# Optimization experiments

Measured on AMD Instinct MI355X. Metric: run time of the kernel, lower is better.

The kernel has to match this reference:

```python
import jax, jax.numpy as jnp
import numpy as np

N1 = 10000; N2 = 10000; F_IN = 256
E_EDGES = 480000; P_PAIRS = 200000
HID = 128; H = 8; DH = 16; L = 2


def _segment_softmax(logits, seg, n):
    # softmax over edges sharing the same destination node (per head)
    m = jax.ops.segment_max(logits, seg, num_segments=n)
    m = jnp.where(jnp.isfinite(m), m, 0.0)
    e = jnp.exp(logits - m[seg])
    s = jax.ops.segment_sum(e, seg, num_segments=n)
    return e / (s[seg] + 1e-16)


def _attend(q_dst, k_src, v_src, src, dst, arel, mrel, prior, n_dst):
    # q_dst: [Nd,H,D]; k_src/v_src: [Ns,H,D]; arel/mrel: [H,D,D]; prior: [H]
    k = jnp.einsum('nhd,hde->nhe', k_src, arel)[src]   # [E,H,D]
    v = jnp.einsum('nhd,hde->nhe', v_src, mrel)[src]   # [E,H,D]
    logits = jnp.einsum('ehd,ehd->eh', q_dst[dst], k) * prior / jnp.sqrt(jnp.asarray(DH, q_dst.dtype))
    a = _segment_softmax(logits, dst, n_dst)           # [E,H]
    out = jax.ops.segment_sum(a[..., None] * v, dst, num_segments=n_dst)
    return out.reshape(n_dst, HID)


def _forward(x_n1, x_n2, Win1, bin1, Win2, bin2, Wk, bk, Wq, bq, Wv, bv, Wa, ba, skip, arel, mrel, prior, ei12, ei21, edge_index):
    proj = lambda x, W, b: (x @ W + b).reshape(-1, H, DH)
    h1 = jax.nn.relu(x_n1 @ Win1 + bin1)
    h2 = jax.nn.relu(x_n2 @ Win2 + bin2)
    feats1, feats2 = [], []
    for l in range(L):
        k1, q1, v1 = proj(h1, Wk[l, 0], bk[l, 0]), proj(h1, Wq[l, 0], bq[l, 0]), proj(h1, Wv[l, 0], bv[l, 0])
        k2, q2, v2 = proj(h2, Wk[l, 1], bk[l, 1]), proj(h2, Wq[l, 1], bq[l, 1]), proj(h2, Wv[l, 1], bv[l, 1])
        # edge type 0: n1 -> n2 (dst = n2); edge type 1: n2 -> n1 (dst = n1)
        agg2 = _attend(q2, k1, v1, ei12[0], ei12[1], arel[l, 0], mrel[l, 0], prior[l, 0], N2)
        agg1 = _attend(q1, k2, v2, ei21[0], ei21[1], arel[l, 1], mrel[l, 1], prior[l, 1], N1)
        o1 = jax.nn.gelu(agg1) @ Wa[l, 0] + ba[l, 0]
        o2 = jax.nn.gelu(agg2) @ Wa[l, 1] + ba[l, 1]
        s1 = jax.nn.sigmoid(skip[l, 0]); s2 = jax.nn.sigmoid(skip[l, 1])
        h1 = s1 * o1 + (1.0 - s1) * h1
        h2 = s2 * o2 + (1.0 - s2) * h2
        feats1.append(h1); feats2.append(h2)
    Em = jnp.concatenate(feats1, axis=1)   # [N1, HID*L]
    Ed = jnp.concatenate(feats2, axis=1)   # [N2, HID*L]
    # scores = Em @ Ed.T then gather at (m_index, d_index); computed as gathered dot
    # products (same math, avoids [N1,N2] materialization). Dropout in eval mode.
    preds = jnp.einsum('pc,pc->p', Em[edge_index[0]], Ed[edge_index[1]])[:, None]
    return preds


def setup_inputs():
    key = jax.random.key(0)
    ks = jax.random.split(key, 16)
    sc = 0.05
    inp = {}
    inp['x_n1'] = jax.random.normal(ks[0], (N1, F_IN), jnp.float32)
    inp['x_n2'] = jax.random.normal(ks[1], (N2, F_IN), jnp.float32)
    inp['ei12'] = jnp.stack([jax.random.randint(ks[2], (E_EDGES,), 0, N1),
                             jax.random.randint(ks[3], (E_EDGES,), 0, N2)])
    inp['ei21'] = jnp.stack([jax.random.randint(ks[4], (E_EDGES,), 0, N2),
                             jax.random.randint(ks[5], (E_EDGES,), 0, N1)])
    inp['edge_index'] = jnp.stack([jax.random.randint(ks[6], (P_PAIRS,), 0, N1),
                                   jax.random.randint(ks[7], (P_PAIRS,), 0, N2)])
    inp['Win1'] = jax.random.normal(ks[8], (F_IN, HID), jnp.float32) * sc
    inp['bin1'] = jnp.zeros((HID,), jnp.float32)
    inp['Win2'] = jax.random.normal(ks[9], (F_IN, HID), jnp.float32) * sc
    inp['bin2'] = jnp.zeros((HID,), jnp.float32)
    inp['Wk'] = jax.random.normal(ks[10], (L, 2, HID, HID), jnp.float32) * sc
    inp['bk'] = jnp.zeros((L, 2, HID), jnp.float32)
    inp['Wq'] = jax.random.normal(ks[11], (L, 2, HID, HID), jnp.float32) * sc
    inp['bq'] = jnp.zeros((L, 2, HID), jnp.float32)
    inp['Wv'] = jax.random.normal(ks[12], (L, 2, HID, HID), jnp.float32) * sc
    inp['bv'] = jnp.zeros((L, 2, HID), jnp.float32)
    inp['Wa'] = jax.random.normal(ks[13], (L, 2, HID, HID), jnp.float32) * sc
    inp['ba'] = jnp.zeros((L, 2, HID), jnp.float32)
    inp['skip'] = jnp.ones((L, 2), jnp.float32)
    inp['arel'] = jax.random.normal(ks[14], (L, 2, H, DH, DH), jnp.float32) * 0.25
    inp['mrel'] = jax.random.normal(ks[15], (L, 2, H, DH, DH), jnp.float32) * 0.25
    inp['prior'] = jnp.ones((L, 2, H), jnp.float32)
    return inp


def reference(x_n1, x_n2, ei12, ei21, edge_index, Win1, bin1, Win2, bin2, Wk, bk, Wq, bq, Wv, bv, Wa, ba, skip, arel, mrel, prior):
    return _forward(x_n1, x_n2, Win1, bin1, Win2, bin2, Wk, bk, Wq, bq, Wv, bv, Wa, ba, skip, arel, mrel, prior, ei12, ei21, edge_index)
```

## Files before the change

kernel.cpp:

```cpp
#include <hip/hip_runtime.h>
#include <math.h>

#define N1c 10000
#define N2c 10000
#define F_INc 256
#define Ec 480000
#define Pc 200000
#define HIDc 128
#define Hc 8
#define DHc 16
#define Lc 2
#define NPART 32
#define NPc 313
#define NBLK 256

using short8 = __attribute__((ext_vector_type(8))) short;
using float4v = __attribute__((ext_vector_type(4))) float;

__device__ __forceinline__ float gelu_f(float x) {
    const float k0 = 0.7978845608028654f;
    const float k1 = 0.044715f;
    float x3 = x * x * x;
    float t = tanhf(k0 * (x + k1 * x3));
    return 0.5f * x * (1.0f + t);
}

__device__ __forceinline__ float bf2f(unsigned short x) {
    union { unsigned int u; float f; } c;
    c.u = ((unsigned int)x) << 16;
    return c.f;
}
__device__ __forceinline__ unsigned short f2bf(float f) {
    union { float f; unsigned int u; } c;
    c.f = f;
    unsigned int u = c.u;
    unsigned int r = (u + 0x7FFFu + ((u >> 16) & 1u)) >> 16;
    return (unsigned short)r;
}

__global__ __launch_bounds__(128) void make_eff_kernel(
    const float* __restrict__ Wq, const float* __restrict__ bq,
    const float* __restrict__ Wk, const float* __restrict__ bk,
    const float* __restrict__ Wv, const float* __restrict__ bv,
    const float* __restrict__ arel, const float* __restrict__ mrel,
    const float* __restrict__ prior,
    short* __restrict__ Wqkvt, float* __restrict__ bqkv)
{
    int col = blockIdx.x * 128 + threadIdx.x;
    int c = blockIdx.y;
    int lt = blockIdx.z;
    short* Wout = Wqkvt + (size_t)lt * 384 * 128;
    float* bout = bqkv + lt * 384;
    if (col < 128) {
        Wout[col * 128 + c] = (short)f2bf(Wq[lt * 16384 + c * 128 + col]);
        if (c == 0) bout[col] = bq[lt * 128 + col];
        return;
    }
    int which = (col < 256) ? 0 : 1;
    int he = col - (which ? 256 : 128);
    int h = he >> 4, e = he & 15;
    const float* W = (which == 0 ? Wk : Wv) + lt * 16384;
    const float* b = (which == 0 ? bk : bv) + lt * 128;
    const float* R = (which == 0 ? arel : mrel) + lt * 2048;
    float sc = (which == 0) ? prior[lt * 8 + h] * 0.25f : 1.0f;
    float acc = 0.f;
    #pragma unroll
    for (int d = 0; d < 16; d++)
        acc += W[c * 128 + h * 16 + d] * R[(h * 16 + d) * 16 + e];
    Wout[col * 128 + c] = (short)f2bf(acc * sc);
    if (c == 0) {
        float bacc = 0.f;
        #pragma unroll
        for (int d = 0; d < 16; d++)
            bacc += b[h * 16 + d] * R[(h * 16 + d) * 16 + e];
        bout[col] = bacc * sc;
    }
}

__global__ __launch_bounds__(256) void wt_prep_kernel(
    const float* __restrict__ Win1, const float* __restrict__ Win2,
    const float* __restrict__ Wa,
    short* __restrict__ Wint1, short* __restrict__ Wint2, short* __restrict__ Wat)
{
    int y = blockIdx.y;
    int id = blockIdx.x * 256 + threadIdx.x;
    if (y < 2) {
        if (id >= 128 * 256) return;
        int n = id >> 8, k = id & 255;
        const float* W = y ? Win2 : Win1;
        short* O = y ? Wint2 : Wint1;
        O[n * 256 + k] = (short)f2bf(W[k * 128 + n]);
    } else {
        if (id >= 128 * 128) return;
        int lt = y - 2;
        int n = id >> 7, k = id & 127;
        Wat[lt * 16384 + n * 128 + k] = (short)f2bf(Wa[lt * 16384 + k * 128 + n]);
    }
}

__global__ __launch_bounds__(256) void count_bins_kernel(
    const int* __restrict__ ei12, const int* __restrict__ ei21, const int* __restrict__ eidx,
    int* __restrict__ cntmat)
{
    int blk = blockIdx.x, z = blockIdx.y, t = threadIdx.x;
    const int* key; int E;
    if (z == 0)      { key = ei12 + Ec; E = Ec; }
    else if (z == 1) { key = ei21 + Ec; E = Ec; }
    else             { key = eidx;      E = Pc; }
    int chunk = (E + NBLK - 1) / NBLK;
    int start = blk * chunk;
    int stop = min(start + chunk, E);
    __shared__ int cnt[NPART];
    if (t < NPART) cnt[t] = 0;
    __syncthreads();
    for (int e = start + t; e < stop; e += 256)
        atomicAdd(&cnt[key[e] / NPc], 1);
    __syncthreads();
    if (t < NPART) cntmat[z * (NPART * NBLK) + t * NBLK + blk] = cnt[t];
}

__global__ __launch_bounds__(256) void scan_bins_kernel(
    const int* __restrict__ cntmat, int* __restrict__ offmat)
{
    int z = blockIdx.x, t = threadIdx.x;
    const int* c = cntmat + z * (NPART * NBLK);
    int* o = offmat + z * (NPART * NBLK);
    int loc[32];
    int base = t * 32;
    int s = 0;
    #pragma unroll
    for (int j = 0; j < 32; j++) { loc[j] = s; s += c[base + j]; }
    __shared__ int ws[256];
    ws[t] = s;
    __syncthreads();
    for (int off = 1; off < 256; off <<= 1) {
        int v = (t >= off) ? ws[t - off] : 0;
        __syncthreads();
        ws[t] += v;
        __syncthreads();
    }
    int excl = t ? ws[t - 1] : 0;
    #pragma unroll
    for (int j = 0; j < 32; j++) o[base + j] = excl + loc[j];
}

__global__ __launch_bounds__(256) void binwrite_kernel(
    const int* __restrict__ ei12, const int* __restrict__ ei21, const int* __restrict__ eidx,
    const int* __restrict__ offmat,
    int2* __restrict__ stg12, int2* __restrict__ stg21, int2* __restrict__ stgm)
{
    int blk = blockIdx.x, z = blockIdx.y, t = threadIdx.x;
    const int* key; const int* pay; int E; int2* stg;
    if (z == 0)      { key = ei12 + Ec; pay = ei12; E = Ec; stg = stg12; }
    else if (z == 1) { key = ei21 + Ec; pay = ei21; E = Ec; stg = stg21; }
    else             { key = eidx;      pay = nullptr; E = Pc; stg = stgm; }
    int chunk = (E + NBLK - 1) / NBLK;
    int start = blk * chunk;
    int stop = min(start + chunk, E);
    const int* om = offmat + z * (NPART * NBLK);
    __shared__ int fill[NPART];
    __shared__ int obase[NPART];
    if (t < NPART) { fill[t] = 0; obase[t] = om[t * NBLK + blk]; }
    __syncthreads();
    for (int e = start + t; e < stop; e += 256) {
        int k = key[e];
        int p = k / NPc;
        int r = atomicAdd(&fill[p], 1);
        stg[obase[p] + r] = make_int2(k, (z == 2) ? e : pay[e]);
    }
}

__global__ __launch_bounds__(256) void build_csr_kernel(
    const int* __restrict__ offmat,
    const int2* __restrict__ stg12, const int2* __restrict__ stg21, const int2* __restrict__ stgm,
    int* __restrict__ rp12, int* __restrict__ rp21, int* __restrict__ rpm,
    int* __restrict__ es12, int* __restrict__ es21, int* __restrict__ ps)
{
    int p = blockIdx.x, z = blockIdx.y, t = threadIdx.x;
    const int2* stg; int* rowptr; int* out; int E;
    if (z == 0)      { stg = stg12; rowptr = rp12; out = es12; E = Ec; }
    else if (z == 1) { stg = stg21; rowptr = rp21; out = es21; E = Ec; }
    else             { stg = stgm;  rowptr = rpm;  out = ps;   E = Pc; }
    const int* om = offmat + z * (NPART * NBLK);
    int base = om[p * NBLK];
    int next = (p == NPART - 1) ? E : om[(p + 1) * NBLK];
    int cntP = next - base;
    int lo = p * NPc;
    int hi = min(lo + NPc, 10000);

    __shared__ int hist[512];
    __shared__ int fill[NPc];
    hist[t] = 0; hist[t + 256] = 0;
    __syncthreads();
    for (int i = t; i < cntP; i += 256)
        atomicAdd(&hist[stg[base + i].x - lo], 1);
    __syncthreads();
    for (int off = 1; off < 512; off <<= 1) {
        int i0 = t, i1 = t + 256;
        int v0 = (i0 >= off) ? hist[i0 - off] : 0;
        int v1 = (i1 >= off) ? hist[i1 - off] : 0;
        __syncthreads();
        hist[i0] += v0; hist[i1] += v1;
        __syncthreads();
    }
    for (int i = t; i < NPc; i += 256) {
        int excl = i ? hist[i - 1] : 0;
        fill[i] = excl;
        if (lo + i < hi) rowptr[lo + i] = base + excl;
    }
    if (p == NPART - 1 && t == 0) rowptr[10000] = E;
    __syncthreads();
    for (int i = t; i < cntP; i += 256) {
        int2 pr = stg[base + i];
        int r = atomicAdd(&fill[pr.x - lo], 1);
        out[base + r] = pr.y;
    }
}

template<int A_GELU, int OUT_RELU, int SKIP, int PACKQKV>
__global__ __launch_bounds__(256) void gemm_mfma(
    const float* __restrict__ A0, const float* __restrict__ A1, int ldA,
    const short* __restrict__ Wt0, const short* __restrict__ Wt1,
    const float* __restrict__ b0, const float* __restrict__ b1,
    float* __restrict__ C0, float* __restrict__ C1, int ldC,
    unsigned short* __restrict__ KV0, unsigned short* __restrict__ KV1,
    int M, int K,
    const float* __restrict__ sk0, const float* __restrict__ sk1,
    const float* __restrict__ H0, const float* __restrict__ H1, int ldH)
{
    int z = blockIdx.z;
    const float* A = z ? A1 : A0;
    const short* Wt = z ? Wt1 : Wt0;
    const float* bias = z ? b1 : b0;
    float* C = z ? C1 : C0;
    unsigned short* KVo = z ? KV1 : KV0;
    const float* skipv = z ? sk1 : sk0;
    const float* Hold = z ? H1 : H0;

    __shared__ short Alds[64 * 40];
    __shared__ short Blds[64 * 40];

    int tid = threadIdx.x;
    int w = tid >> 6;
    int l = tid & 63;
    int mBase = blockIdx.x * 64;
    int nBase = blockIdx.y * 64;

    int srow = tid >> 2;
    int koct = tid & 3;

    float4v acc[4];
    #pragma unroll
    for (int i = 0; i < 4; i++) acc[i] = (float4v){0.f, 0.f, 0.f, 0.f};

    int arow = mBase + srow;
    const float* Aptr = A + (size_t)arow * ldA + koct * 8;
    const short* Wptr = Wt + (size_t)(nBase + srow) * K + koct * 8;

    int fl = l & 15;
    int fo = (l >> 4) * 8;

    for (int k0 = 0; k0 < K; k0 += 32) {
        float av[8];
        if (arow < M) {
            const float4* p = (const float4*)(Aptr + k0);
            float4 f0 = p[0], f1 = p[1];
            av[0] = f0.x; av[1] = f0.y; av[2] = f0.z; av[3] = f0.w;
            av[4] = f1.x; av[5] = f1.y; av[6] = f1.z; av[7] = f1.w;
        } else {
            #pragma unroll
            for (int i = 0; i < 8; i++) av[i] = 0.f;
        }
        if (A_GELU) {
            #pragma unroll
            for (int i = 0; i < 8; i++) av[i] = gelu_f(av[i]);
        }
        unsigned int pk[4];
        #pragma unroll
        for (int i = 0; i < 4; i++)
            pk[i] = (unsigned int)f2bf(av[2 * i]) | ((unsigned int)f2bf(av[2 * i + 1]) << 16);
        *(uint4*)&Alds[srow * 40 + koct * 8] = make_uint4(pk[0], pk[1], pk[2], pk[3]);
        *(uint4*)&Blds[srow * 40 + koct * 8] = *(const uint4*)(Wptr + k0);
        __syncthreads();

        short8 bfr = *(const short8*)&Blds[(w * 16 + fl) * 40 + fo];
        #pragma unroll
        for (int msub = 0; msub < 4; msub++) {
            short8 afr = *(const short8*)&Alds[(msub * 16 + fl) * 40 + fo];
            acc[msub] = __builtin_amdgcn_mfma_f32_16x16x32_bf16(afr, bfr, acc[msub], 0, 0, 0);
        }
        __syncthreads();
    }

    float sig = 0.f;
    if (SKIP) sig = 1.f / (1.f + __expf(-skipv[0]));
    int col = nBase + w * 16 + fl;
    float bcol = bias[col];
    int rbase = mBase + ((l >> 4) * 4);
    #pragma unroll
    for (int msub = 0; msub < 4; msub++) {
        #pragma unroll
        for (int r = 0; r < 4; r++) {
            int row = rbase + msub * 16 + r;
            if (row >= M) continue;
            float v = acc[msub][r] + bcol;
            if (OUT_RELU) v = fmaxf(v, 0.f);
            if (SKIP) v = sig * v + (1.f - sig) * Hold[(size_t)row * ldH + col];
            if (PACKQKV) {
                if (col < 128) C[(size_t)row * ldC + col] = v;
                else KVo[(size_t)row * 256 + (col - 128)] = f2bf(v);
            } else {
                C[(size_t)row * ldC + col] = v;
            }
        }
    }
}

__device__ __forceinline__ float4 bfv4(ushort4 u) {
    return make_float4(bf2f(u.x), bf2f(u.y), bf2f(u.z), bf2f(u.w));
}

__global__ __launch_bounds__(256) void attend2_kernel(
    const float* __restrict__ Q1, const unsigned short* __restrict__ KV1,
    const float* __restrict__ Q2, const unsigned short* __restrict__ KV2,
    const int* __restrict__ rp12, const int* __restrict__ es12,
    const int* __restrict__ rp21, const int* __restrict__ es21,
    float* __restrict__ agg1, float* __restrict__ agg2)
{
    int g = blockIdx.x * 8 + (threadIdx.x >> 5);
    int l = threadIdx.x & 31;
    const float* Q; const unsigned short* KV; const int* rp; const int* es; float* out; int n;
    if (g < N2c) { n = g;       Q = Q2; KV = KV1; rp = rp12; es = es12; out = agg2; }
    else         { n = g - N2c; Q = Q1; KV = KV2; rp = rp21; es = es21; out = agg1; }

    float4 q = *(const float4*)(Q + (size_t)n * 128 + 4 * l);
    int beg = rp[n], end = rp[n + 1];
    float s0 = 0.f, s1 = 0.f, s2 = 0.f, s3 = 0.f;
    float4 a0 = {0,0,0,0}, a1 = {0,0,0,0}, a2 = {0,0,0,0}, a3 = {0,0,0,0};
    int i = beg;
    for (; i + 4 <= end; i += 4) {
        int e0 = es[i], e1 = es[i+1], e2 = es[i+2], e3 = es[i+3];
        const unsigned short* r0 = KV + (size_t)e0 * 256 + 4 * l;
        const unsigned short* r1 = KV + (size_t)e1 * 256 + 4 * l;
        const unsigned short* r2 = KV + (size_t)e2 * 256 + 4 * l;
        const unsigned short* r3 = KV + (size_t)e3 * 256 + 4 * l;
        float4 k0 = bfv4(*(const ushort4*)r0), v0 = bfv4(*(const ushort4*)(r0 + 128));
        float4 k1 = bfv4(*(const ushort4*)r1), v1 = bfv4(*(const ushort4*)(r1 + 128));
        float4 k2 = bfv4(*(const ushort4*)r2), v2 = bfv4(*(const ushort4*)(r2 + 128));
        float4 k3 = bfv4(*(const ushort4*)r3), v3 = bfv4(*(const ushort4*)(r3 + 128));
        float p0 = q.x*k0.x + q.y*k0.y + q.z*k0.z + q.w*k0.w;
        float p1 = q.x*k1.x + q.y*k1.y + q.z*k1.z + q.w*k1.w;
        float p2 = q.x*k2.x + q.y*k2.y + q.z*k2.z + q.w*k2.w;
        float p3 = q.x*k3.x + q.y*k3.y + q.z*k3.z + q.w*k3.w;
        p0 += __shfl_xor(p0, 1, 4); p1 += __shfl_xor(p1, 1, 4);
        p2 += __shfl_xor(p2, 1, 4); p3 += __shfl_xor(p3, 1, 4);
        p0 += __shfl_xor(p0, 2, 4); p1 += __shfl_xor(p1, 2, 4);
        p2 += __shfl_xor(p2, 2, 4); p3 += __shfl_xor(p3, 2, 4);
        float x0 = __expf(p0), x1 = __expf(p1), x2 = __expf(p2), x3 = __expf(p3);
        s0 += x0; s1 += x1; s2 += x2; s3 += x3;
        a0.x += x0*v0.x; a0.y += x0*v0.y; a0.z += x0*v0.z; a0.w += x0*v0.w;
        a1.x += x1*v1.x; a1.y += x1*v1.y; a1.z += x1*v1.z; a1.w += x1*v1.w;
        a2.x += x2*v2.x; a2.y += x2*v2.y; a2.z += x2*v2.z; a2.w += x2*v2.w;
        a3.x += x3*v3.x; a3.y += x3*v3.y; a3.z += x3*v3.z; a3.w += x3*v3.w;
    }
    for (; i < end; i++) {
        int e0 = es[i];
        const unsigned short* r0 = KV + (size_t)e0 * 256 + 4 * l;
        float4 k0 = bfv4(*(const ushort4*)r0), v0 = bfv4(*(const ushort4*)(r0 + 128));
        float p0 = q.x*k0.x + q.y*k0.y + q.z*k0.z + q.w*k0.w;
        p0 += __shfl_xor(p0, 1, 4);
        p0 += __shfl_xor(p0, 2, 4);
        float x0 = __expf(p0);
        s0 += x0;
        a0.x += x0*v0.x; a0.y += x0*v0.y; a0.z += x0*v0.z; a0.w += x0*v0.w;
    }
    float ssum = (s0 + s1) + (s2 + s3);
    float inv = 1.f / (ssum + 1e-16f);
    float4 o;
    o.x = ((a0.x + a1.x) + (a2.x + a3.x)) * inv;
    o.y = ((a0.y + a1.y) + (a2.y + a3.y)) * inv;
    o.z = ((a0.z + a1.z) + (a2.z + a3.z)) * inv;
    o.w = ((a0.w + a1.w) + (a2.w + a3.w)) * inv;
    *(float4*)(out + (size_t)n * 128 + 4 * l) = o;
}

__global__ __launch_bounds__(256) void pred_kernel(
    const float* __restrict__ Em, const float* __restrict__ Ed,
    const int* __restrict__ eidx,
    const int* __restrict__ rpm, const int* __restrict__ porder,
    float* __restrict__ out)
{
    int m = blockIdx.x * 4 + (threadIdx.x >> 6);
    int lane = threadIdx.x & 63;
    int beg = rpm[m], end = rpm[m + 1];
    if (beg == end) return;
    float4 a = *(const float4*)(Em + (size_t)m * 256 + 4 * lane);
    int i = beg;
    for (; i + 2 <= end; i += 2) {
        int p0 = porder[i], p1 = porder[i + 1];
        int d0 = eidx[Pc + p0], d1 = eidx[Pc + p1];
        float4 b0 = *(const float4*)(Ed + (size_t)d0 * 256 + 4 * lane);
        float4 b1 = *(const float4*)(Ed + (size_t)d1 * 256 + 4 * lane);
        float s0 = a.x*b0.x + a.y*b0.y + a.z*b0.z + a.w*b0.w;
        float s1 = a.x*b1.x + a.y*b1.y + a.z*b1.z + a.w*b1.w;
        #pragma unroll
        for (int o = 1; o < 64; o <<= 1) { s0 += __shfl_xor(s0, o); s1 += __shfl_xor(s1, o); }
        if (lane == 0) { out[p0] = s0; out[p1] = s1; }
    }
    if (i < end) {
        int p0 = porder[i];
        int d0 = eidx[Pc + p0];
        float4 b0 = *(const float4*)(Ed + (size_t)d0 * 256 + 4 * lane);
        float s0 = a.x*b0.x + a.y*b0.y + a.z*b0.z + a.w*b0.w;
        #pragma unroll
        for (int o = 1; o < 64; o <<= 1) s0 += __shfl_xor(s0, o);
        if (lane == 0) out[p0] = s0;
    }
}

extern "C" void kernel_launch(void* const* d_in, const int* in_sizes, int n_in,
                              void* d_out, int out_size, void* d_ws, size_t ws_size,
                              hipStream_t stream)
{
    const float* x1   = (const float*)d_in[0];
    const float* x2   = (const float*)d_in[1];
    const int*   ei12 = (const int*)d_in[2];
    const int*   ei21 = (const int*)d_in[3];
    const int*   eidx = (const int*)d_in[4];
    const float* Win1 = (const float*)d_in[5];
    const float* bin1 = (const float*)d_in[6];
    const float* Win2 = (const float*)d_in[7];
    const float* bin2 = (const float*)d_in[8];
    const float* Wk   = (const float*)d_in[9];
    const float* bk   = (const float*)d_in[10];
    const float* Wq   = (const float*)d_in[11];
    const float* bq   = (const float*)d_in[12];
    const float* Wv   = (const float*)d_in[13];
    const float* bv   = (const float*)d_in[14];
    const float* Wa   = (const float*)d_in[15];
    const float* ba   = (const float*)d_in[16];
    const float* skip = (const float*)d_in[17];
    const float* arel = (const float*)d_in[18];
    const float* mrel = (const float*)d_in[19];
    const float* prior= (const float*)d_in[20];

    char* ws = (char*)d_ws;
    size_t off = 0;
    auto allocB = [&](size_t bytes) { void* p = ws + off; off += (bytes + 15) & ~15ull; return p; };
    auto allocF = [&](size_t n) { return (float*)allocB(n * 4); };
    auto allocI = [&](size_t n) { return (int*)allocB(n * 4); };
    auto allocS = [&](size_t n) { return (short*)allocB(n * 2); };

    float* h1    = allocF((size_t)N1c * 128);
    float* h2    = allocF((size_t)N2c * 128);
    float* Q1    = allocF((size_t)N1c * 128);
    float* Q2    = allocF((size_t)N2c * 128);
    float* agg1  = allocF((size_t)N1c * 128);
    float* agg2  = allocF((size_t)N2c * 128);
    float* Em    = allocF((size_t)N1c * 256);
    float* Ed    = allocF((size_t)N2c * 256);
    float* bqkv  = allocF(4 * 384);
    short* Wqkvt = allocS(4 * 384 * 128);
    short* Wint1 = allocS(128 * 256);
    short* Wint2 = allocS(128 * 256);
    short* Wat   = allocS(4 * 128 * 128);
    unsigned short* KV1 = (unsigned short*)allocS((size_t)N1c * 256);
    unsigned short* KV2 = (unsigned short*)allocS((size_t)N2c * 256);
    int* rp12  = allocI(N2c + 1);
    int* rp21  = allocI(N1c + 1);
    int* rpm   = allocI(N1c + 1);
    int* es12  = allocI(Ec);
    int* es21  = allocI(Ec);
    int* ps    = allocI(Pc);
    int* cntmat = allocI(3 * NPART * NBLK);
    int* offmat = allocI(3 * NPART * NBLK);
    int2* stg12 = (int2*)allocB((size_t)Ec * 8);
    int2* stg21 = (int2*)allocB((size_t)Ec * 8);
    int2* stgm  = (int2*)allocB((size_t)Pc * 8);

    make_eff_kernel<<<dim3(3, 128, 4), 128, 0, stream>>>(
        Wq, bq, Wk, bk, Wv, bv, arel, mrel, prior, Wqkvt, bqkv);
    wt_prep_kernel<<<dim3(128, 6), 256, 0, stream>>>(Win1, Win2, Wa, Wint1, Wint2, Wat);

    count_bins_kernel<<<dim3(NBLK, 3), 256, 0, stream>>>(ei12, ei21, eidx, cntmat);
    scan_bins_kernel<<<3, 256, 0, stream>>>(cntmat, offmat);
    binwrite_kernel<<<dim3(NBLK, 3), 256, 0, stream>>>(ei12, ei21, eidx, offmat,
                                                       stg12, stg21, stgm);
    build_csr_kernel<<<dim3(NPART, 3), 256, 0, stream>>>(offmat, stg12, stg21, stgm,
                                                         rp12, rp21, rpm, es12, es21, ps);

    const int MB = (N1c + 63) / 64;
    gemm_mfma<0, 1, 0, 0><<<dim3(MB, 2, 2), 256, 0, stream>>>(
        x1, x2, F_INc, Wint1, Wint2, bin1, bin2, h1, h2, 128,
        nullptr, nullptr,
        N1c, F_INc, nullptr, nullptr, nullptr, nullptr, 0);

    for (int l = 0; l < Lc; l++) {
        const float* A1 = (l == 0) ? h1 : Em;  int ld1 = (l == 0) ? 128 : 256;
        const float* A2 = (l == 0) ? h2 : Ed;
        int lt0 = l * 2 + 0, lt1 = l * 2 + 1;
        gemm_mfma<0, 0, 0, 1><<<dim3(MB, 6, 2), 256, 0, stream>>>(
            A1, A2, ld1,
            Wqkvt + (size_t)lt0 * 49152, Wqkvt + (size_t)lt1 * 49152,
            bqkv + lt0 * 384, bqkv + lt1 * 384,
            Q1, Q2, 128,
            KV1, KV2,
            N1c, 128,
            nullptr, nullptr, nullptr, nullptr, 0);
        attend2_kernel<<<(N1c + N2c) / 8, 256, 0, stream>>>(
            Q1, KV1, Q2, KV2, rp12, es12, rp21, es21, agg1, agg2);
        gemm_mfma<1, 0, 1, 0><<<dim3(MB, 2, 2), 256, 0, stream>>>(
            agg1, agg2, 128,
            Wat + (size_t)lt0 * 16384, Wat + (size_t)lt1 * 16384,
            ba + lt0 * 128, ba + lt1 * 128,
            Em + l * 128, Ed + l * 128, 256,
            nullptr, nullptr,
            N1c, 128,
            skip + lt0, skip + lt1,
            A1, A2, ld1);
    }

    pred_kernel<<<N1c / 4, 256, 0, stream>>>(Em, Ed, eidx, rpm, ps, (float*)d_out);
}
```

Before: 361.2 us.

## Split attention per node into two half-feature 16-lane groups and vectorize edge index loads

The attention kernel now assigns each destination node to two 16-lane groups, each handling 64 of the 128 feature columns (four heads), in separate blocks ordered by job phase. Edge-index reads in the unrolled loop become a single aligned int4 load, with a scalar prologue added to reach 4-element alignment. This doubles the number of concurrent gather streams and cuts per-thread instruction overhead on index loads. In exchange, the edge list and row pointers are read twice, and each K/V row fetch covers only half a row.

```diff
diff --git a/kernel.cpp b/kernel.cpp
--- a/kernel.cpp
+++ b/kernel.cpp
@@ -327,23 +327,39 @@
     const int* __restrict__ rp21, const int* __restrict__ es21,
     float* __restrict__ agg1, float* __restrict__ agg2)
 {
-    int g = blockIdx.x * 8 + (threadIdx.x >> 5);
-    int l = threadIdx.x & 31;
-    const float* Q; const unsigned short* KV; const int* rp; const int* es; float* out; int n;
-    if (g < N2c) { n = g;       Q = Q2; KV = KV1; rp = rp12; es = es12; out = agg2; }
-    else         { n = g - N2c; Q = Q1; KV = KV2; rp = rp21; es = es21; out = agg1; }
-
-    float4 q = *(const float4*)(Q + (size_t)n * 128 + 4 * l);
+    int job = blockIdx.x / 625;
+    int n = (blockIdx.x % 625) * 16 + (threadIdx.x >> 4);
+    int ln = threadIdx.x & 15;
+    int phase = job & 1;
+    const float* Q; const unsigned short* KV; const int* rp; const int* es; float* out;
+    if (job < 2) { Q = Q2; KV = KV1; rp = rp12; es = es12; out = agg2; }
+    else         { Q = Q1; KV = KV2; rp = rp21; es = es21; out = agg1; }
+    int co = phase * 64 + 4 * ln;
+
+    float4 q = *(const float4*)(Q + (size_t)n * 128 + co);
+    const unsigned short* KVc = KV + co;
     int beg = rp[n], end = rp[n + 1];
     float s0 = 0.f, s1 = 0.f, s2 = 0.f, s3 = 0.f;
     float4 a0 = {0,0,0,0}, a1 = {0,0,0,0}, a2 = {0,0,0,0}, a3 = {0,0,0,0};
+
     int i = beg;
+    int pre = min(end, (beg + 3) & ~3);
+    for (; i < pre; i++) {
+        const unsigned short* r0 = KVc + (size_t)es[i] * 256;
+        float4 k0 = bfv4(*(const ushort4*)r0), v0 = bfv4(*(const ushort4*)(r0 + 128));
+        float p0 = q.x*k0.x + q.y*k0.y + q.z*k0.z + q.w*k0.w;
+        p0 += __shfl_xor(p0, 1, 4);
+        p0 += __shfl_xor(p0, 2, 4);
+        float x0 = __expf(p0);
+        s0 += x0;
+        a0.x += x0*v0.x; a0.y += x0*v0.y; a0.z += x0*v0.z; a0.w += x0*v0.w;
+    }
     for (; i + 4 <= end; i += 4) {
-        int e0 = es[i], e1 = es[i+1], e2 = es[i+2], e3 = es[i+3];
-        const unsigned short* r0 = KV + (size_t)e0 * 256 + 4 * l;
-        const unsigned short* r1 = KV + (size_t)e1 * 256 + 4 * l;
-        const unsigned short* r2 = KV + (size_t)e2 * 256 + 4 * l;
-        const unsigned short* r3 = KV + (size_t)e3 * 256 + 4 * l;
+        int4 e = *(const int4*)&es[i];
+        const unsigned short* r0 = KVc + (size_t)e.x * 256;
+        const unsigned short* r1 = KVc + (size_t)e.y * 256;
+        const unsigned short* r2 = KVc + (size_t)e.z * 256;
+        const unsigned short* r3 = KVc + (size_t)e.w * 256;
         float4 k0 = bfv4(*(const ushort4*)r0), v0 = bfv4(*(const ushort4*)(r0 + 128));
         float4 k1 = bfv4(*(const ushort4*)r1), v1 = bfv4(*(const ushort4*)(r1 + 128));
         float4 k2 = bfv4(*(const ushort4*)r2), v2 = bfv4(*(const ushort4*)(r2 + 128));
@@ -364,8 +380,7 @@
         a3.x += x3*v3.x; a3.y += x3*v3.y; a3.z += x3*v3.z; a3.w += x3*v3.w;
     }
     for (; i < end; i++) {
-        int e0 = es[i];
-        const unsigned short* r0 = KV + (size_t)e0 * 256 + 4 * l;
+        const unsigned short* r0 = KVc + (size_t)es[i] * 256;
         float4 k0 = bfv4(*(const ushort4*)r0), v0 = bfv4(*(const ushort4*)(r0 + 128));
         float p0 = q.x*k0.x + q.y*k0.y + q.z*k0.z + q.w*k0.w;
         p0 += __shfl_xor(p0, 1, 4);
@@ -381,7 +396,7 @@
     o.y = ((a0.y + a1.y) + (a2.y + a3.y)) * inv;
     o.z = ((a0.z + a1.z) + (a2.z + a3.z)) * inv;
     o.w = ((a0.w + a1.w) + (a2.w + a3.w)) * inv;
-    *(float4*)(out + (size_t)n * 128 + 4 * l) = o;
+    *(float4*)(out + (size_t)n * 128 + co) = o;
 }
 
 __global__ __launch_bounds__(256) void pred_kernel(
@@ -507,7 +522,7 @@
             KV1, KV2,
             N1c, 128,
             nullptr, nullptr, nullptr, nullptr, 0);
-        attend2_kernel<<<(N1c + N2c) / 8, 256, 0, stream>>>(
+        attend2_kernel<<<2500, 256, 0, stream>>>(
             Q1, KV1, Q2, KV2, rp12, es12, rp21, es21, agg1, agg2);
         gemm_mfma<1, 0, 1, 0><<<dim3(MB, 2, 2), 256, 0, stream>>>(
             agg1, agg2, 128,
```

Result: no change. 364.9 us (+1.0%).

## Store keys in fp8 and Ed in bf16, reshape attention to 16-lane groups

Applied to the files above, without the earlier changes.

The QKV GEMM epilogue now writes keys as fp8 and values as separate bf16 arrays, and the attention kernel reads these narrower rows with 16 lanes per node and 8 elements per lane. The combined attention launch is split into two launches, one per edge type. The output GEMM also writes a bf16 copy of Ed, which the prediction kernel gathers instead of fp32. The aim is to cut gather bandwidth in the memory-bound attention and prediction kernels, at the cost of lower precision on keys and on the score path. K is also made a template parameter so the GEMM loop can be fully unrolled.

```diff
diff --git a/kernel.cpp b/kernel.cpp
--- a/kernel.cpp
+++ b/kernel.cpp
@@ -16,6 +16,7 @@
 
 using short8 = __attribute__((ext_vector_type(8))) short;
 using float4v = __attribute__((ext_vector_type(4))) float;
+using floatx2 = __attribute__((ext_vector_type(2))) float;
 
 __device__ __forceinline__ float gelu_f(float x) {
     const float k0 = 0.7978845608028654f;
@@ -36,6 +37,10 @@
     unsigned int u = c.u;
     unsigned int r = (u + 0x7FFFu + ((u >> 16) & 1u)) >> 16;
     return (unsigned short)r;
+}
+__device__ __forceinline__ unsigned char f2fp8(float v) {
+    unsigned int p = __builtin_amdgcn_cvt_pk_fp8_f32(v, v, 0u, false);
+    return (unsigned char)(p & 0xFF);
 }
 
 __global__ __launch_bounds__(128) void make_eff_kernel(
@@ -217,14 +222,16 @@
     }
 }
 
-template<int A_GELU, int OUT_RELU, int SKIP, int PACKQKV>
+template<int A_GELU, int OUT_RELU, int SKIP, int PACKQKV, int EXB, int KT>
 __global__ __launch_bounds__(256) void gemm_mfma(
     const float* __restrict__ A0, const float* __restrict__ A1, int ldA,
     const short* __restrict__ Wt0, const short* __restrict__ Wt1,
     const float* __restrict__ b0, const float* __restrict__ b1,
     float* __restrict__ C0, float* __restrict__ C1, int ldC,
-    unsigned short* __restrict__ KV0, unsigned short* __restrict__ KV1,
-    int M, int K,
+    unsigned char* __restrict__ K8o0, unsigned char* __restrict__ K8o1,
+    unsigned short* __restrict__ Vb0, unsigned short* __restrict__ Vb1,
+    unsigned short* __restrict__ EX0, unsigned short* __restrict__ EX1,
+    int M,
     const float* __restrict__ sk0, const float* __restrict__ sk1,
     const float* __restrict__ H0, const float* __restrict__ H1, int ldH)
 {
@@ -233,7 +240,9 @@
     const short* Wt = z ? Wt1 : Wt0;
     const float* bias = z ? b1 : b0;
     float* C = z ? C1 : C0;
-    unsigned short* KVo = z ? KV1 : KV0;
+    unsigned char* K8o = z ? K8o1 : K8o0;
+    unsigned short* Vbo = z ? Vb1 : Vb0;
+    unsigned short* EX = z ? EX1 : EX0;
     const float* skipv = z ? sk1 : sk0;
     const float* Hold = z ? H1 : H0;
 
@@ -255,12 +264,13 @@
 
     int arow = mBase + srow;
     const float* Aptr = A + (size_t)arow * ldA + koct * 8;
-    const short* Wptr = Wt + (size_t)(nBase + srow) * K + koct * 8;
+    const short* Wptr = Wt + (size_t)(nBase + srow) * KT + koct * 8;
 
     int fl = l & 15;
     int fo = (l >> 4) * 8;
 
-    for (int k0 = 0; k0 < K; k0 += 32) {
+    #pragma unroll
+    for (int k0 = 0; k0 < KT; k0 += 32) {
         float av[8];
         if (arow < M) {
             const float4* p = (const float4*)(Aptr + k0);
@@ -308,84 +318,103 @@
             if (SKIP) v = sig * v + (1.f - sig) * Hold[(size_t)row * ldH + col];
             if (PACKQKV) {
                 if (col < 128) C[(size_t)row * ldC + col] = v;
-                else KVo[(size_t)row * 256 + (col - 128)] = f2bf(v);
+                else if (col < 256) K8o[(size_t)row * 128 + (col - 128)] = f2fp8(v);
+                else Vbo[(size_t)row * 128 + (col - 256)] = f2bf(v);
             } else {
                 C[(size_t)row * ldC + col] = v;
+                if (EXB && EX) EX[(size_t)row * 256 + col] = f2bf(v);
             }
         }
     }
 }
 
-__device__ __forceinline__ float4 bfv4(ushort4 u) {
-    return make_float4(bf2f(u.x), bf2f(u.y), bf2f(u.z), bf2f(u.w));
-}
-
-__global__ __launch_bounds__(256) void attend2_kernel(
-    const float* __restrict__ Q1, const unsigned short* __restrict__ KV1,
-    const float* __restrict__ Q2, const unsigned short* __restrict__ KV2,
-    const int* __restrict__ rp12, const int* __restrict__ es12,
-    const int* __restrict__ rp21, const int* __restrict__ es21,
-    float* __restrict__ agg1, float* __restrict__ agg2)
-{
-    int g = blockIdx.x * 8 + (threadIdx.x >> 5);
-    int l = threadIdx.x & 31;
-    const float* Q; const unsigned short* KV; const int* rp; const int* es; float* out; int n;
-    if (g < N2c) { n = g;       Q = Q2; KV = KV1; rp = rp12; es = es12; out = agg2; }
-    else         { n = g - N2c; Q = Q1; KV = KV2; rp = rp21; es = es21; out = agg1; }
-
-    float4 q = *(const float4*)(Q + (size_t)n * 128 + 4 * l);
+__global__ __launch_bounds__(256) void attend_kernel(
+    const float* __restrict__ Q, const unsigned char* __restrict__ K8,
+    const unsigned short* __restrict__ Vb,
+    const int* __restrict__ rp, const int* __restrict__ es,
+    float* __restrict__ out)
+{
+    int n = blockIdx.x * 16 + (threadIdx.x >> 4);
+    int ln = threadIdx.x & 15;
+
+    float q[8];
+    {
+        const float4* qp = (const float4*)(Q + (size_t)n * 128 + 8 * ln);
+        float4 q0 = qp[0], q1 = qp[1];
+        q[0]=q0.x; q[1]=q0.y; q[2]=q0.z; q[3]=q0.w;
+        q[4]=q1.x; q[5]=q1.y; q[6]=q1.z; q[7]=q1.w;
+    }
     int beg = rp[n], end = rp[n + 1];
-    float s0 = 0.f, s1 = 0.f, s2 = 0.f, s3 = 0.f;
-    float4 a0 = {0,0,0,0}, a1 = {0,0,0,0}, a2 = {0,0,0,0}, a3 = {0,0,0,0};
+    float s = 0.f;
+    float acc[8];
+    #pragma unroll
+    for (int c = 0; c < 8; c++) acc[c] = 0.f;
+
+    auto edge_kv = [&](int e, float* kd, float* vd) {
+        const unsigned char* kr = K8 + (size_t)e * 128 + 8 * ln;
+        uint2 kw = *(const uint2*)kr;
+        floatx2 k01 = __builtin_amdgcn_cvt_pk_f32_fp8(kw.x, false);
+        floatx2 k23 = __builtin_amdgcn_cvt_pk_f32_fp8(kw.x, true);
+        floatx2 k45 = __builtin_amdgcn_cvt_pk_f32_fp8(kw.y, false);
+        floatx2 k67 = __builtin_amdgcn_cvt_pk_f32_fp8(kw.y, true);
+        kd[0]=k01[0]; kd[1]=k01[1]; kd[2]=k23[0]; kd[3]=k23[1];
+        kd[4]=k45[0]; kd[5]=k45[1]; kd[6]=k67[0]; kd[7]=k67[1];
+        const ushort4* vr = (const ushort4*)(Vb + (size_t)e * 128 + 8 * ln);
+        ushort4 v0 = vr[0], v1 = vr[1];
+        vd[0]=bf2f(v0.x); vd[1]=bf2f(v0.y); vd[2]=bf2f(v0.z); vd[3]=bf2f(v0.w);
+        vd[4]=bf2f(v1.x); vd[5]=bf2f(v1.y); vd[6]=bf2f(v1.z); vd[7]=bf2f(v1.w);
+    };
+    auto dot8 = [&](const float* kd) {
+        float p = q[0]*kd[0] + q[1]*kd[1] + q[2]*kd[2] + q[3]*kd[3]
+                + q[4]*kd[4] + q[5]*kd[5] + q[6]*kd[6] + q[7]*kd[7];
+        p += __shfl_xor(p, 1, 2);
+        return p;
+    };
+
     int i = beg;
+    int pre = min(end, (beg + 3) & ~3);
+    for (; i < pre; i++) {
+        float kd[8], vd[8];
+        edge_kv(es[i], kd, vd);
+        float x = __expf(dot8(kd));
+        s += x;
+        #pragma unroll
+        for (int c = 0; c < 8; c++) acc[c] += x * vd[c];
+    }
     for (; i + 4 <= end; i += 4) {
-        int e0 = es[i], e1 = es[i+1], e2 = es[i+2], e3 = es[i+3];
-        const unsigned short* r0 = KV + (size_t)e0 * 256 + 4 * l;
-        const unsigned short* r1 = KV + (size_t)e1 * 256 + 4 * l;
-        const unsigned short* r2 = KV + (size_t)e2 * 256 + 4 * l;
-        const unsigned short* r3 = KV + (size_t)e3 * 256 + 4 * l;
-        float4 k0 = bfv4(*(const ushort4*)r0), v0 = bfv4(*(const ushort4*)(r0 + 128));
-        float4 k1 = bfv4(*(const ushort4*)r1), v1 = bfv4(*(const ushort4*)(r1 + 128));
-        float4 k2 = bfv4(*(const ushort4*)r2), v2 = bfv4(*(const ushort4*)(r2 + 128));
-        float4 k3 = bfv4(*(const ushort4*)r3), v3 = bfv4(*(const ushort4*)(r3 + 128));
-        float p0 = q.x*k0.x + q.y*k0.y + q.z*k0.z + q.w*k0.w;
-        float p1 = q.x*k1.x + q.y*k1.y + q.z*k1.z + q.w*k1.w;
-        float p2 = q.x*k2.x + q.y*k2.y + q.z*k2.z + q.w*k2.w;
-        float p3 = q.x*k3.x + q.y*k3.y + q.z*k3.z + q.w*k3.w;
-        p0 += __shfl_xor(p0, 1, 4); p1 += __shfl_xor(p1, 1, 4);
-        p2 += __shfl_xor(p2, 1, 4); p3 += __shfl_xor(p3, 1, 4);
-        p0 += __shfl_xor(p0, 2, 4); p1 += __shfl_xor(p1, 2, 4);
-        p2 += __shfl_xor(p2, 2, 4); p3 += __shfl_xor(p3, 2, 4);
-        float x0 = __expf(p0), x1 = __expf(p1), x2 = __expf(p2), x3 = __expf(p3);
-        s0 += x0; s1 += x1; s2 += x2; s3 += x3;
-        a0.x += x0*v0.x; a0.y += x0*v0.y; a0.z += x0*v0.z; a0.w += x0*v0.w;
-        a1.x += x1*v1.x; a1.y += x1*v1.y; a1.z += x1*v1.z; a1.w += x1*v1.w;
-        a2.x += x2*v2.x; a2.y += x2*v2.y; a2.z += x2*v2.z; a2.w += x2*v2.w;
-        a3.x += x3*v3.x; a3.y += x3*v3.y; a3.z += x3*v3.z; a3.w += x3*v3.w;
+        int4 e = *(const int4*)&es[i];
+        float k0[8], v0[8], k1[8], v1[8], k2[8], v2[8], k3[8], v3[8];
+        edge_kv(e.x, k0, v0);
+        edge_kv(e.y, k1, v1);
+        edge_kv(e.z, k2, v2);
+        edge_kv(e.w, k3, v3);
+        float x0 = __expf(dot8(k0));
+        float x1 = __expf(dot8(k1));
+        float x2 = __expf(dot8(k2));
+        float x3 = __expf(dot8(k3));
+        s += (x0 + x1) + (x2 + x3);
+        #pragma unroll
+        for (int c = 0; c < 8; c++)
+            acc[c] += x0 * v0[c] + x1 * v1[c] + x2 * v2[c] + x3 * v3[c];
     }
     for (; i < end; i++) {
-        int e0 = es[i];
-        const unsigned short* r0 = KV + (size_t)e0 * 256 + 4 * l;
-        float4 k0 = bfv4(*(const ushort4*)r0), v0 = bfv4(*(const ushort4*)(r0 + 128));
-        float p0 = q.x*k0.x + q.y*k0.y + q.z*k0.z + q.w*k0.w;
-        p0 += __shfl_xor(p0, 1, 4);
-        p0 += __shfl_xor(p0, 2, 4);
-        float x0 = __expf(p0);
-        s0 += x0;
-        a0.x += x0*v0.x; a0.y += x0*v0.y; a0.z += x0*v0.z; a0.w += x0*v0.w;
-    }
-    float ssum = (s0 + s1) + (s2 + s3);
-    float inv = 1.f / (ssum + 1e-16f);
-    float4 o;
-    o.x = ((a0.x + a1.x) + (a2.x + a3.x)) * inv;
-    o.y = ((a0.y + a1.y) + (a2.y + a3.y)) * inv;
-    o.z = ((a0.z + a1.z) + (a2.z + a3.z)) * inv;
-    o.w = ((a0.w + a1.w) + (a2.w + a3.w)) * inv;
-    *(float4*)(out + (size_t)n * 128 + 4 * l) = o;
+        float kd[8], vd[8];
+        edge_kv(es[i], kd, vd);
+        float x = __expf(dot8(kd));
+        s += x;
+        #pragma unroll
+        for (int c = 0; c < 8; c++) acc[c] += x * vd[c];
+    }
+
+    float inv = 1.f / (s + 1e-16f);
+    float4 o0 = make_float4(acc[0]*inv, acc[1]*inv, acc[2]*inv, acc[3]*inv);
+    float4 o1 = make_float4(acc[4]*inv, acc[5]*inv, acc[6]*inv, acc[7]*inv);
+    float4* op = (float4*)(out + (size_t)n * 128 + 8 * ln);
+    op[0] = o0; op[1] = o1;
 }
 
 __global__ __launch_bounds__(256) void pred_kernel(
-    const float* __restrict__ Em, const float* __restrict__ Ed,
+    const float* __restrict__ Em, const unsigned short* __restrict__ Edb,
     const int* __restrict__ eidx,
     const int* __restrict__ rpm, const int* __restrict__ porder,
     float* __restrict__ out)
@@ -399,10 +428,10 @@
     for (; i + 2 <= end; i += 2) {
         int p0 = porder[i], p1 = porder[i + 1];
         int d0 = eidx[Pc + p0], d1 = eidx[Pc + p1];
-        float4 b0 = *(const float4*)(Ed + (size_t)d0 * 256 + 4 * lane);
-        float4 b1 = *(const float4*)(Ed + (size_t)d1 * 256 + 4 * lane);
-        float s0 = a.x*b0.x + a.y*b0.y + a.z*b0.z + a.w*b0.w;
-        float s1 = a.x*b1.x + a.y*b1.y + a.z*b1.z + a.w*b1.w;
+        ushort4 u0 = *(const ushort4*)(Edb + (size_t)d0 * 256 + 4 * lane);
+        ushort4 u1 = *(const ushort4*)(Edb + (size_t)d1 * 256 + 4 * lane);
+        float s0 = a.x*bf2f(u0.x) + a.y*bf2f(u0.y) + a.z*bf2f(u0.z) + a.w*bf2f(u0.w);
+        float s1 = a.x*bf2f(u1.x) + a.y*bf2f(u1.y) + a.z*bf2f(u1.z) + a.w*bf2f(u1.w);
         #pragma unroll
         for (int o = 1; o < 64; o <<= 1) { s0 += __shfl_xor(s0, o); s1 += __shfl_xor(s1, o); }
         if (lane == 0) { out[p0] = s0; out[p1] = s1; }
@@ -410,8 +439,8 @@
     if (i < end) {
         int p0 = porder[i];
         int d0 = eidx[Pc + p0];
-        float4 b0 = *(const float4*)(Ed + (size_t)d0 * 256 + 4 * lane);
-        float s0 = a.x*b0.x + a.y*b0.y + a.z*b0.z + a.w*b0.w;
+        ushort4 u0 = *(const ushort4*)(Edb + (size_t)d0 * 256 + 4 * lane);
+        float s0 = a.x*bf2f(u0.x) + a.y*bf2f(u0.y) + a.z*bf2f(u0.z) + a.w*bf2f(u0.w);
         #pragma unroll
         for (int o = 1; o < 64; o <<= 1) s0 += __shfl_xor(s0, o);
         if (lane == 0) out[p0] = s0;
@@ -464,8 +493,11 @@
     short* Wint1 = allocS(128 * 256);
     short* Wint2 = allocS(128 * 256);
     short* Wat   = allocS(4 * 128 * 128);
-    unsigned short* KV1 = (unsigned short*)allocS((size_t)N1c * 256);
-    unsigned short* KV2 = (unsigned short*)allocS((size_t)N2c * 256);
+    unsigned char*  K81 = (unsigned char*)allocB((size_t)N1c * 128);
+    unsigned char*  K82 = (unsigned char*)allocB((size_t)N2c * 128);
+    unsigned short* Vb1 = (unsigned short*)allocS((size_t)N1c * 128);
+    unsigned short* Vb2 = (unsigned short*)allocS((size_t)N2c * 128);
+    unsigned short* Edb = (unsigned short*)allocS((size_t)N2c * 256);
     int* rp12  = allocI(N2c + 1);
     int* rp21  = allocI(N1c + 1);
     int* rpm   = allocI(N1c + 1);
@@ -490,35 +522,35 @@
                                                          rp12, rp21, rpm, es12, es21, ps);
 
     const int MB = (N1c + 63) / 64;
-    gemm_mfma<0, 1, 0, 0><<<dim3(MB, 2, 2), 256, 0, stream>>>(
+    gemm_mfma<0, 1, 0, 0, 0, 256><<<dim3(MB, 2, 2), 256, 0, stream>>>(
         x1, x2, F_INc, Wint1, Wint2, bin1, bin2, h1, h2, 128,
-        nullptr, nullptr,
-        N1c, F_INc, nullptr, nullptr, nullptr, nullptr, 0);
+        nullptr, nullptr, nullptr, nullptr, nullptr, nullptr,
+        N1c, nullptr, nullptr, nullptr, nullptr, 0);
 
     for (int l = 0; l < Lc; l++) {
         const float* A1 = (l == 0) ? h1 : Em;  int ld1 = (l == 0) ? 128 : 256;
         const float* A2 = (l == 0) ? h2 : Ed;
         int lt0 = l * 2 + 0, lt1 = l * 2 + 1;
-        gemm_mfma<0, 0, 0, 1><<<dim3(MB, 6, 2), 256, 0, stream>>>(
+        gemm_mfma<0, 0, 0, 1, 0, 128><<<dim3(MB, 6, 2), 256, 0, stream>>>(
             A1, A2, ld1,
             Wqkvt + (size_t)lt0 * 49152, Wqkvt + (size_t)lt1 * 49152,
             bqkv + lt0 * 384, bqkv + lt1 * 384,
             Q1, Q2, 128,
-            KV1, KV2,
-            N1c, 128,
-            nullptr, nullptr, nullptr, nullptr, 0);
-        attend2_kernel<<<(N1c + N2c) / 8, 256, 0, stream>>>(
-            Q1, KV1, Q2, KV2, rp12, es12, rp21, es21, agg1, agg2);
-        gemm_mfma<1, 0, 1, 0><<<dim3(MB, 2, 2), 256, 0, stream>>>(
+            K81, K82, Vb1, Vb2, nullptr, nullptr,
+            N1c, nullptr, nullptr, nullptr, nullptr, 0);
+        attend_kernel<<<N2c / 16, 256, 0, stream>>>(Q2, K81, Vb1, rp12, es12, agg2);
+        attend_kernel<<<N1c / 16, 256, 0, stream>>>(Q1, K82, Vb2, rp21, es21, agg1);
+        gemm_mfma<1, 0, 1, 0, 1, 128><<<dim3(MB, 2, 2), 256, 0, stream>>>(
             agg1, agg2, 128,
             Wat + (size_t)lt0 * 16384, Wat + (size_t)lt1 * 16384,
             ba + lt0 * 128, ba + lt1 * 128,
             Em + l * 128, Ed + l * 128, 256,
-            nullptr, nullptr,
-            N1c, 128,
+            nullptr, nullptr, nullptr, nullptr,
+            nullptr, Edb + l * 128,
+            N1c,
             skip + lt0, skip + lt1,
             A1, A2, ld1);
     }
 
-    pred_kernel<<<N1c / 4, 256, 0, stream>>>(Em, Ed, eidx, rpm, ps, (float*)d_out);
-}
+    pred_kernel<<<N1c / 4, 256, 0, stream>>>(Em, Edb, eidx, rpm, ps, (float*)d_out);
+}
```

Measured after the change: 363.4 us. Within noise of the previous version (+0.6%).
